# Optimization experiments

Hardware: AMD Instinct MI355X
Metric: run time of the kernel (lower is better)

The kernel has to match this reference:

```python
import jax, jax.numpy as jnp
import numpy as np

EPS = 1e-12  # tf.math.l2_normalize epsilon

def l2norm(x):
    # tf.math.l2_normalize: x * rsqrt(max(sum(x^2), eps)) along last axis
    sq = jnp.sum(x * x, axis=-1, keepdims=True)
    return x * jax.lax.rsqrt(jnp.maximum(sq, EPS))

def setup_inputs() -> dict:
    key = jax.random.key(0)
    ks = jax.random.split(key, 10)
    B, L, D = 2, 512, 256
    OD = 256
    return {
        "queries": jax.random.normal(ks[0], (B, L, D), jnp.float32),
        "keys": jax.random.normal(ks[1], (B, L, D), jnp.float32),
        "values": jax.random.normal(ks[2], (B, L, D), jnp.float32),
        "relative_encoding_lookup": jax.random.normal(ks[3], (B, L, L, OD), jnp.float32),
        "edge_type_embedding": jax.random.normal(ks[4], (B, L, L, OD), jnp.float32),
        "Wq": jax.random.normal(ks[5], (D, OD), jnp.float32) * 0.05,
        "bq": jnp.zeros((OD,), jnp.float32),
        "Wk": jax.random.normal(ks[6], (D, OD), jnp.float32) * 0.05,
        "bk": jnp.zeros((OD,), jnp.float32),
        "Wv": jax.random.normal(ks[7], (D, OD), jnp.float32) * 0.05,
        "bv": jnp.zeros((OD,), jnp.float32),
    }

def reference(queries, keys, values, relative_encoding_lookup, edge_type_embedding,
              Wq, bq, Wk, bk, Wv, bv):
    d = queries.shape[-1]  # NOTE: original uses the INPUT dim (pre-projection) for scaling
    q = l2norm(jnp.matmul(queries, Wq) + bq)   # [B,L,OD]
    k = l2norm(jnp.matmul(keys, Wk) + bk)      # [B,L,OD]
    v = l2norm(jnp.matmul(values, Wv) + bv)    # [B,L,OD]
    scores_qk = jnp.einsum('bld,bmd->blm', q, k) * 0.4
    # Original broadcasts q to [B,L,L,OD] then multiply+reduce; expressed here as a
    # batched contraction (same math, no [B,L,L,OD] query broadcast materialized).
    # NOTE: the original computes scores_position (*0.2) but then overwrites it:
    #   scores = scores_ + scores_position; scores = scores_ + scores_edge_embedding
    # so scores_position is dead code and does NOT affect the output.
    scores_edge = jnp.einsum('bld,blmd->blm', q, edge_type_embedding) * 0.6
    inv_sqrt_d = jax.lax.rsqrt(jnp.float32(d))
    scores = (scores_qk + scores_edge) * inv_sqrt_d
    return scores, v, q
```

## Files before the change

### kernel.cpp

```cpp
#include <hip/hip_runtime.h>

#define SEQ_L 512
#define DIM 256

typedef float f4 __attribute__((ext_vector_type(4)));

__global__ __launch_bounds__(256) void proj_norm3_kernel(
    const float* __restrict__ Xq, const float* __restrict__ Wq,
    const float* __restrict__ bq, float* __restrict__ oq,
    const float* __restrict__ Xk, const float* __restrict__ Wk,
    const float* __restrict__ bk, float* __restrict__ ok,
    const float* __restrict__ Xv, const float* __restrict__ Wv,
    const float* __restrict__ bv, float* __restrict__ ov)
{
    const float* X; const float* W; const float* bias; float* out;
    if (blockIdx.y == 0)      { X = Xq; W = Wq; bias = bq; out = oq; }
    else if (blockIdx.y == 1) { X = Xk; W = Wk; bias = bk; out = ok; }
    else                      { X = Xv; W = Wv; bias = bv; out = ov; }

    const int ROWS = 8;
    __shared__ float xs[ROWS][DIM];
    __shared__ float red[ROWS][4];

    const int t  = threadIdx.x;
    const int r0 = blockIdx.x * ROWS;

    #pragma unroll
    for (int r = 0; r < ROWS; ++r)
        xs[r][t] = X[(size_t)(r0 + r) * DIM + t];
    __syncthreads();

    const float b = bias[t];
    float acc[ROWS];
    #pragma unroll
    for (int r = 0; r < ROWS; ++r) acc[r] = b;

    for (int d = 0; d < DIM; ++d) {
        const float wv = W[(size_t)d * DIM + t];
        #pragma unroll
        for (int r = 0; r < ROWS; ++r)
            acc[r] += xs[r][d] * wv;
    }

    const int lane = t & 63;
    const int wid  = t >> 6;

    #pragma unroll
    for (int r = 0; r < ROWS; ++r) {
        float ss = acc[r] * acc[r];
        #pragma unroll
        for (int off = 32; off >= 1; off >>= 1)
            ss += __shfl_down(ss, off, 64);
        if (lane == 0) red[r][wid] = ss;
    }
    __syncthreads();

    #pragma unroll
    for (int r = 0; r < ROWS; ++r) {
        const float s = red[r][0] + red[r][1] + red[r][2] + red[r][3];
        const float scale = rsqrtf(fmaxf(s, 1e-12f));
        out[(size_t)(r0 + r) * DIM + t] = acc[r] * scale;
    }
}

__global__ __launch_bounds__(256) void qk4_kernel(
    const float* __restrict__ q, const float* __restrict__ k,
    float* __restrict__ out)
{
    const int l0    = blockIdx.x * 4;
    const int b     = l0 >> 9;
    const int lane  = threadIdx.x & 63;
    const int wave  = threadIdx.x >> 6;
    const int m_sub = lane & 7;
    const int d_sub = lane >> 3;

    f4 qf[4][8];
    #pragma unroll
    for (int r = 0; r < 4; ++r) {
        const f4* q4 = (const f4*)(q + (size_t)(l0 + r) * DIM);
        #pragma unroll
        for (int c = 0; c < 8; ++c) qf[r][c] = q4[c * 8 + d_sub];
    }

    const f4* k4 = (const f4*)(k + (size_t)b * SEQ_L * DIM);

    for (int m0 = wave * 8; m0 < SEQ_L; m0 += 32) {
        const size_t base = (size_t)(m0 + m_sub) * (DIM / 4) + d_sub;
        f4 kf[8];
        #pragma unroll
        for (int c = 0; c < 8; ++c) kf[c] = k4[base + c * 8];

        #pragma unroll
        for (int r = 0; r < 4; ++r) {
            float sa = 0.f, sb = 0.f;
            #pragma unroll
            for (int c = 0; c < 8; ++c) {
                sa += qf[r][c].x * kf[c].x + qf[r][c].y * kf[c].y;
                sb += qf[r][c].z * kf[c].z + qf[r][c].w * kf[c].w;
            }
            float s = sa + sb;
            s += __shfl_xor(s, 8, 64);
            s += __shfl_xor(s, 16, 64);
            s += __shfl_xor(s, 32, 64);
            if (lane < 8)
                out[(size_t)(l0 + r) * SEQ_L + m0 + lane] = s * 0.025f;
        }
    }
}

__global__ __launch_bounds__(256) void edge_kernel(
    const float* __restrict__ q, const float* __restrict__ edge,
    float* __restrict__ out)
{
    const int bl    = blockIdx.x;
    const int lane  = threadIdx.x & 63;
    const int wave  = threadIdx.x >> 6;
    const int m_sub = lane & 7;
    const int d_sub = lane >> 3;

    const f4* q4 = (const f4*)(q + (size_t)bl * DIM);
    f4 qf[8];
    #pragma unroll
    for (int c = 0; c < 8; ++c) qf[c] = q4[c * 8 + d_sub];

    const f4* e4 = (const f4*)(edge + (size_t)bl * SEQ_L * DIM);
    float* orow = out + (size_t)bl * SEQ_L;

    const int mbase = blockIdx.y * 256;
    for (int m0 = mbase + wave * 8; m0 < mbase + 256; m0 += 64) {
        const int m1 = m0 + 32;
        const size_t ba0 = (size_t)(m0 + m_sub) * (DIM / 4) + d_sub;
        const size_t ba1 = (size_t)(m1 + m_sub) * (DIM / 4) + d_sub;

        f4 e0[8], e1[8];
        #pragma unroll
        for (int c = 0; c < 8; ++c) {
            e0[c] = __builtin_nontemporal_load(&e4[ba0 + c * 8]);
            e1[c] = __builtin_nontemporal_load(&e4[ba1 + c * 8]);
        }

        float base0 = 0.f, base1 = 0.f;
        if (lane < 8) { base0 = orow[m0 + lane]; base1 = orow[m1 + lane]; }

        float sa0 = 0.f, sb0 = 0.f, sa1 = 0.f, sb1 = 0.f;
        #pragma unroll
        for (int c = 0; c < 8; ++c) {
            sa0 += qf[c].x * e0[c].x + qf[c].y * e0[c].y;
            sb0 += qf[c].z * e0[c].z + qf[c].w * e0[c].w;
            sa1 += qf[c].x * e1[c].x + qf[c].y * e1[c].y;
            sb1 += qf[c].z * e1[c].z + qf[c].w * e1[c].w;
        }
        float s0 = sa0 + sb0, s1 = sa1 + sb1;
        s0 += __shfl_xor(s0, 8, 64);  s1 += __shfl_xor(s1, 8, 64);
        s0 += __shfl_xor(s0, 16, 64); s1 += __shfl_xor(s1, 16, 64);
        s0 += __shfl_xor(s0, 32, 64); s1 += __shfl_xor(s1, 32, 64);

        if (lane < 8) {
            orow[m0 + lane] = fmaf(s0, 0.0375f, base0);
            orow[m1 + lane] = fmaf(s1, 0.0375f, base1);
        }
    }
}

extern "C" void kernel_launch(void* const* d_in, const int* in_sizes, int n_in,
                              void* d_out, int out_size, void* d_ws, size_t ws_size,
                              hipStream_t stream) {
    const float* queries = (const float*)d_in[0];
    const float* keys    = (const float*)d_in[1];
    const float* values  = (const float*)d_in[2];
    const float* edge    = (const float*)d_in[4];
    const float* Wq = (const float*)d_in[5];
    const float* bq = (const float*)d_in[6];
    const float* Wk = (const float*)d_in[7];
    const float* bk = (const float*)d_in[8];
    const float* Wv = (const float*)d_in[9];
    const float* bv = (const float*)d_in[10];

    float* out = (float*)d_out;

    const int B = in_sizes[0] / (SEQ_L * DIM);
    const size_t scores_sz = (size_t)B * SEQ_L * SEQ_L;
    const size_t qkv_sz    = (size_t)B * SEQ_L * DIM;

    float* v_out = out + scores_sz;
    float* q_out = out + scores_sz + qkv_sz;
    float* k_ws  = (float*)d_ws;

    const int rows = B * SEQ_L;

    dim3 pgrid(rows / 8, 3);
    proj_norm3_kernel<<<pgrid, 256, 0, stream>>>(
        queries, Wq, bq, q_out,
        keys,    Wk, bk, k_ws,
        values,  Wv, bv, v_out);

    qk4_kernel<<<rows / 4, 256, 0, stream>>>(q_out, k_ws, out);

    dim3 egrid(rows, 2);
    edge_kernel<<<egrid, 256, 0, stream>>>(q_out, edge, out);
}
```

Before: 127.3 us.

## Software-pipeline edge loads with double buffering and vectorize projection LDS reads

```diff
diff --git a/kernel.cpp b/kernel.cpp
--- a/kernel.cpp
+++ b/kernel.cpp
@@ -19,7 +19,7 @@
     else                      { X = Xv; W = Wv; bias = bv; out = ov; }
 
     const int ROWS = 8;
-    __shared__ float xs[ROWS][DIM];
+    __shared__ __align__(16) float xs[ROWS][DIM];
     __shared__ float red[ROWS][4];
 
     const int t  = threadIdx.x;
@@ -35,11 +35,16 @@
     #pragma unroll
     for (int r = 0; r < ROWS; ++r) acc[r] = b;
 
-    for (int d = 0; d < DIM; ++d) {
-        const float wv = W[(size_t)d * DIM + t];
-        #pragma unroll
-        for (int r = 0; r < ROWS; ++r)
-            acc[r] += xs[r][d] * wv;
+    for (int d4 = 0; d4 < DIM / 4; ++d4) {
+        const float w0 = W[(size_t)(d4 * 4 + 0) * DIM + t];
+        const float w1 = W[(size_t)(d4 * 4 + 1) * DIM + t];
+        const float w2 = W[(size_t)(d4 * 4 + 2) * DIM + t];
+        const float w3 = W[(size_t)(d4 * 4 + 3) * DIM + t];
+        #pragma unroll
+        for (int r = 0; r < ROWS; ++r) {
+            const f4 xv = ((const f4*)xs[r])[d4];
+            acc[r] += xv.x * w0 + xv.y * w1 + xv.z * w2 + xv.w * w3;
+        }
     }
 
     const int lane = t & 63;
@@ -126,40 +131,42 @@
     const f4* e4 = (const f4*)(edge + (size_t)bl * SEQ_L * DIM);
     float* orow = out + (size_t)bl * SEQ_L;
 
-    const int mbase = blockIdx.y * 256;
-    for (int m0 = mbase + wave * 8; m0 < mbase + 256; m0 += 64) {
-        const int m1 = m0 + 32;
-        const size_t ba0 = (size_t)(m0 + m_sub) * (DIM / 4) + d_sub;
-        const size_t ba1 = (size_t)(m1 + m_sub) * (DIM / 4) + d_sub;
-
-        f4 e0[8], e1[8];
-        #pragma unroll
-        for (int c = 0; c < 8; ++c) {
-            e0[c] = __builtin_nontemporal_load(&e4[ba0 + c * 8]);
-            e1[c] = __builtin_nontemporal_load(&e4[ba1 + c * 8]);
-        }
-
-        float base0 = 0.f, base1 = 0.f;
-        if (lane < 8) { base0 = orow[m0 + lane]; base1 = orow[m1 + lane]; }
-
-        float sa0 = 0.f, sb0 = 0.f, sa1 = 0.f, sb1 = 0.f;
-        #pragma unroll
-        for (int c = 0; c < 8; ++c) {
-            sa0 += qf[c].x * e0[c].x + qf[c].y * e0[c].y;
-            sb0 += qf[c].z * e0[c].z + qf[c].w * e0[c].w;
-            sa1 += qf[c].x * e1[c].x + qf[c].y * e1[c].y;
-            sb1 += qf[c].z * e1[c].z + qf[c].w * e1[c].w;
-        }
-        float s0 = sa0 + sb0, s1 = sa1 + sb1;
-        s0 += __shfl_xor(s0, 8, 64);  s1 += __shfl_xor(s1, 8, 64);
-        s0 += __shfl_xor(s0, 16, 64); s1 += __shfl_xor(s1, 16, 64);
-        s0 += __shfl_xor(s0, 32, 64); s1 += __shfl_xor(s1, 32, 64);
-
-        if (lane < 8) {
-            orow[m0 + lane] = fmaf(s0, 0.0375f, base0);
-            orow[m1 + lane] = fmaf(s1, 0.0375f, base1);
-        }
-    }
+    f4 eA[8], eB[8];
+    float baseA, baseB;
+    const int mw = wave * 8;
+
+#define LOADG(BUF, BASEV, MI) do {                                          \
+        const size_t ba_ = (size_t)((MI) + m_sub) * (DIM / 4) + d_sub;      \
+        _Pragma("unroll")                                                   \
+        for (int c_ = 0; c_ < 8; ++c_) BUF[c_] = e4[ba_ + c_ * 8];          \
+        BASEV = (lane < 8) ? orow[(MI) + lane] : 0.f;                       \
+    } while (0)
+
+#define COMPG(BUF, BASEV, MI) do {                                          \
+        float sa_ = 0.f, sb_ = 0.f;                                         \
+        _Pragma("unroll")                                                   \
+        for (int c_ = 0; c_ < 8; ++c_) {                                    \
+            sa_ += qf[c_].x * BUF[c_].x + qf[c_].y * BUF[c_].y;             \
+            sb_ += qf[c_].z * BUF[c_].z + qf[c_].w * BUF[c_].w;             \
+        }                                                                   \
+        float s_ = sa_ + sb_;                                               \
+        s_ += __shfl_xor(s_, 8, 64);                                        \
+        s_ += __shfl_xor(s_, 16, 64);                                       \
+        s_ += __shfl_xor(s_, 32, 64);                                       \
+        if (lane < 8) orow[(MI) + lane] = fmaf(s_, 0.0375f, BASEV);         \
+    } while (0)
+
+    LOADG(eA, baseA, mw + 0 * 32);
+    #pragma unroll
+    for (int i = 0; i < 8; ++i) {
+        LOADG(eB, baseB, mw + (2 * i + 1) * 32);
+        COMPG(eA, baseA, mw + (2 * i) * 32);
+        if (i < 7) LOADG(eA, baseA, mw + (2 * i + 2) * 32);
+        COMPG(eB, baseB, mw + (2 * i + 1) * 32);
+    }
+
+#undef LOADG
+#undef COMPG
 }
 
 extern "C" void kernel_launch(void* const* d_in, const int* in_sizes, int n_in,
@@ -196,6 +203,5 @@
 
     qk4_kernel<<<rows / 4, 256, 0, stream>>>(q_out, k_ws, out);
 
-    dim3 egrid(rows, 2);
-    edge_kernel<<<egrid, 256, 0, stream>>>(q_out, edge, out);
-}
+    edge_kernel<<<rows, 256, 0, stream>>>(q_out, edge, out);
+}
```

Result: slower. 164.0 us (+28.9%).

## Fuse QK score computation into edge kernel and vectorize projection LDS reads

Applied to the files above, without the earlier changes.

```diff
diff --git a/kernel.cpp b/kernel.cpp
--- a/kernel.cpp
+++ b/kernel.cpp
@@ -19,7 +19,7 @@
     else                      { X = Xv; W = Wv; bias = bv; out = ov; }
 
     const int ROWS = 8;
-    __shared__ float xs[ROWS][DIM];
+    __shared__ __align__(16) float xs[ROWS][DIM];
     __shared__ float red[ROWS][4];
 
     const int t  = threadIdx.x;
@@ -35,11 +35,17 @@
     #pragma unroll
     for (int r = 0; r < ROWS; ++r) acc[r] = b;
 
-    for (int d = 0; d < DIM; ++d) {
-        const float wv = W[(size_t)d * DIM + t];
+    #pragma unroll 2
+    for (int d4 = 0; d4 < DIM / 4; ++d4) {
+        const float w0 = W[(size_t)(d4 * 4 + 0) * DIM + t];
+        const float w1 = W[(size_t)(d4 * 4 + 1) * DIM + t];
+        const float w2 = W[(size_t)(d4 * 4 + 2) * DIM + t];
+        const float w3 = W[(size_t)(d4 * 4 + 3) * DIM + t];
         #pragma unroll
-        for (int r = 0; r < ROWS; ++r)
-            acc[r] += xs[r][d] * wv;
+        for (int r = 0; r < ROWS; ++r) {
+            const f4 xv = ((const f4*)xs[r])[d4];
+            acc[r] += xv.x * w0 + xv.y * w1 + xv.z * w2 + xv.w * w3;
+        }
     }
 
     const int lane = t & 63;
@@ -63,71 +69,50 @@
     }
 }
 
-__global__ __launch_bounds__(256) void qk4_kernel(
+__global__ __launch_bounds__(256) void qk_edge_kernel(
     const float* __restrict__ q, const float* __restrict__ k,
-    float* __restrict__ out)
+    const float* __restrict__ edge, float* __restrict__ out)
 {
-    const int l0    = blockIdx.x * 4;
-    const int b     = l0 >> 9;
+    const int bl    = blockIdx.x;
+    const int b     = bl >> 9;
     const int lane  = threadIdx.x & 63;
     const int wave  = threadIdx.x >> 6;
     const int m_sub = lane & 7;
     const int d_sub = lane >> 3;
-
-    f4 qf[4][8];
-    #pragma unroll
-    for (int r = 0; r < 4; ++r) {
-        const f4* q4 = (const f4*)(q + (size_t)(l0 + r) * DIM);
-        #pragma unroll
-        for (int c = 0; c < 8; ++c) qf[r][c] = q4[c * 8 + d_sub];
-    }
-
-    const f4* k4 = (const f4*)(k + (size_t)b * SEQ_L * DIM);
-
-    for (int m0 = wave * 8; m0 < SEQ_L; m0 += 32) {
-        const size_t base = (size_t)(m0 + m_sub) * (DIM / 4) + d_sub;
-        f4 kf[8];
-        #pragma unroll
-        for (int c = 0; c < 8; ++c) kf[c] = k4[base + c * 8];
-
-        #pragma unroll
-        for (int r = 0; r < 4; ++r) {
-            float sa = 0.f, sb = 0.f;
-            #pragma unroll
-            for (int c = 0; c < 8; ++c) {
-                sa += qf[r][c].x * kf[c].x + qf[r][c].y * kf[c].y;
-                sb += qf[r][c].z * kf[c].z + qf[r][c].w * kf[c].w;
-            }
-            float s = sa + sb;
-            s += __shfl_xor(s, 8, 64);
-            s += __shfl_xor(s, 16, 64);
-            s += __shfl_xor(s, 32, 64);
-            if (lane < 8)
-                out[(size_t)(l0 + r) * SEQ_L + m0 + lane] = s * 0.025f;
-        }
-    }
-}
-
-__global__ __launch_bounds__(256) void edge_kernel(
-    const float* __restrict__ q, const float* __restrict__ edge,
-    float* __restrict__ out)
-{
-    const int bl    = blockIdx.x;
-    const int lane  = threadIdx.x & 63;
-    const int wave  = threadIdx.x >> 6;
-    const int m_sub = lane & 7;
-    const int d_sub = lane >> 3;
+    const int mw    = blockIdx.y * 128 + wave * 8;
 
     const f4* q4 = (const f4*)(q + (size_t)bl * DIM);
     f4 qf[8];
     #pragma unroll
     for (int c = 0; c < 8; ++c) qf[c] = q4[c * 8 + d_sub];
 
+    const f4* k4 = (const f4*)(k + (size_t)b * SEQ_L * DIM);
     const f4* e4 = (const f4*)(edge + (size_t)bl * SEQ_L * DIM);
     float* orow = out + (size_t)bl * SEQ_L;
 
-    const int mbase = blockIdx.y * 256;
-    for (int m0 = mbase + wave * 8; m0 < mbase + 256; m0 += 64) {
+    float qkr[4];
+    #pragma unroll
+    for (int g = 0; g < 4; ++g) {
+        const size_t ba = (size_t)(mw + g * 32 + m_sub) * (DIM / 4) + d_sub;
+        f4 kf[8];
+        #pragma unroll
+        for (int c = 0; c < 8; ++c) kf[c] = k4[ba + c * 8];
+        float sa = 0.f, sb = 0.f;
+        #pragma unroll
+        for (int c = 0; c < 8; ++c) {
+            sa += qf[c].x * kf[c].x + qf[c].y * kf[c].y;
+            sb += qf[c].z * kf[c].z + qf[c].w * kf[c].w;
+        }
+        float s = sa + sb;
+        s += __shfl_xor(s, 8, 64);
+        s += __shfl_xor(s, 16, 64);
+        s += __shfl_xor(s, 32, 64);
+        qkr[g] = s * 0.025f;
+    }
+
+    #pragma unroll
+    for (int i = 0; i < 2; ++i) {
+        const int m0 = mw + i * 64;
         const int m1 = m0 + 32;
         const size_t ba0 = (size_t)(m0 + m_sub) * (DIM / 4) + d_sub;
         const size_t ba1 = (size_t)(m1 + m_sub) * (DIM / 4) + d_sub;
@@ -138,9 +123,6 @@
             e0[c] = __builtin_nontemporal_load(&e4[ba0 + c * 8]);
             e1[c] = __builtin_nontemporal_load(&e4[ba1 + c * 8]);
         }
-
-        float base0 = 0.f, base1 = 0.f;
-        if (lane < 8) { base0 = orow[m0 + lane]; base1 = orow[m1 + lane]; }
 
         float sa0 = 0.f, sb0 = 0.f, sa1 = 0.f, sb1 = 0.f;
         #pragma unroll
@@ -156,8 +138,8 @@
         s0 += __shfl_xor(s0, 32, 64); s1 += __shfl_xor(s1, 32, 64);
 
         if (lane < 8) {
-            orow[m0 + lane] = fmaf(s0, 0.0375f, base0);
-            orow[m1 + lane] = fmaf(s1, 0.0375f, base1);
+            orow[m0 + lane] = fmaf(s0, 0.0375f, qkr[2 * i]);
+            orow[m1 + lane] = fmaf(s1, 0.0375f, qkr[2 * i + 1]);
         }
     }
 }
@@ -194,8 +176,6 @@
         keys,    Wk, bk, k_ws,
         values,  Wv, bv, v_out);
 
-    qk4_kernel<<<rows / 4, 256, 0, stream>>>(q_out, k_ws, out);
-
-    dim3 egrid(rows, 2);
-    edge_kernel<<<egrid, 256, 0, stream>>>(q_out, edge, out);
+    dim3 egrid(rows, 4);
+    qk_edge_kernel<<<egrid, 256, 0, stream>>>(q_out, k_ws, edge, out);
 }
```

Measured after the change: 148.5 us. 1.17x slower.
